# Kernel optimization log

Measured on AMD Instinct MI355X. Metric: run time of the kernel, lower is better.

## Reference

```python
import jax, jax.numpy as jnp
from jax import lax
import numpy as np

D_MODEL = 512
D_STATE = 16
DI = 1024        # expand * d_model
DT_RANK = 32     # ceil(d_model/16)
K = 4            # mamba d_conv
NC = 8           # n_clusters
B = 2
L = 1024
EPS_LN = 1e-5


def _ln(x, g, b):
    m = jnp.mean(x, axis=-1, keepdims=True)
    v = jnp.mean((x - m) ** 2, axis=-1, keepdims=True)
    return (x - m) / jnp.sqrt(v + EPS_LN) * g + b


def _l2norm(x):
    n = jnp.linalg.norm(x, axis=-1, keepdims=True)
    return x / jnp.maximum(n, 1e-12)


def _ssm_scan(dA, dBu, C):
    # dA, dBu: (B, L, DI, N); C: (B, L, N) -> y: (B, L, DI)
    def step(h, inp):
        dA_t, dBu_t, c_t = inp
        h = dA_t * h + dBu_t                      # (B, DI, N)
        y = jnp.einsum('bdn,bn->bd', h, c_t)      # (B, DI)
        return h, y
    h0 = jnp.zeros((dA.shape[0], dA.shape[2], dA.shape[3]), dA.dtype)
    _, ys = lax.scan(step, h0, (jnp.swapaxes(dA, 0, 1), jnp.swapaxes(dBu, 0, 1), jnp.swapaxes(C, 0, 1)))
    return jnp.swapaxes(ys, 0, 1)


def _mamba(x, in_w, conv_w, conv_b, xproj_w, dt_w, dt_b, A_log, Dp, out_w):
    # x: (B, L, d_model)
    xz = x @ in_w.T                               # (B, L, 2*DI)
    xp, z = jnp.split(xz, 2, axis=-1)
    # depthwise causal conv1d
    xc = lax.conv_general_dilated(jnp.swapaxes(xp, 1, 2), conv_w, (1,), [(K - 1, 0)], feature_group_count=DI)
    xc = jax.nn.silu(xc + conv_b[None, :, None])
    xc = jnp.swapaxes(xc, 1, 2)                   # (B, L, DI)
    x_dbl = xc @ xproj_w.T                        # (B, L, DT_RANK + 2*N)
    dt, Bm, Cm = jnp.split(x_dbl, [DT_RANK, DT_RANK + D_STATE], axis=-1)
    delta = jax.nn.softplus(dt @ dt_w.T + dt_b)   # (B, L, DI)
    A = -jnp.exp(A_log)                           # (DI, N)
    dA = jnp.exp(delta[..., None] * A)            # (B, L, DI, N)
    dBu = (delta * xc)[..., None] * Bm[:, :, None, :]
    y = _ssm_scan(dA, dBu, Cm) + xc * Dp
    y = y * jax.nn.silu(z)
    return y @ out_w.T


def _forward(x, norm1_g, norm1_b,
             fm_in_w, fm_conv_w, fm_conv_b, fm_xproj_w, fm_dt_w, fm_dt_b, fm_A_log, fm_D, fm_out_w,
             bm_in_w, bm_conv_w, bm_conv_b, bm_xproj_w, bm_dt_w, bm_dt_b, bm_A_log, bm_D, bm_out_w,
             fusion_w, fusion_b, cc_centers, cc_proj_w, cc_proj_b, cc_norm_g, cc_norm_b, cc_alpha,
             gate_w, gate_b, ffn_norm_g, ffn_norm_b, ffn_w1, ffn_b1, ffn_w2, ffn_b2):
    xn = _ln(x, norm1_g, norm1_b)
    # bidirectional mamba path
    f_out = _mamba(xn, fm_in_w, fm_conv_w, fm_conv_b, fm_xproj_w, fm_dt_w, fm_dt_b, fm_A_log, fm_D, fm_out_w)
    b_out = jnp.flip(_mamba(jnp.flip(xn, axis=1), bm_in_w, bm_conv_w, bm_conv_b, bm_xproj_w, bm_dt_w, bm_dt_b, bm_A_log, bm_D, bm_out_w), axis=1)
    mamba_out = jnp.concatenate([f_out, b_out], axis=-1) @ fusion_w.T + fusion_b
    # context clustering path (dropout = identity at eval)
    proj = xn @ cc_proj_w.T + cc_proj_b
    sim = jnp.einsum('bld,cd->blc', _l2norm(proj), _l2norm(cc_centers))
    w = jax.nn.softmax(sim, axis=-1)
    ctx = jnp.einsum('blc,cd->bld', w, cc_centers)
    cc_out = _ln(xn + cc_alpha * ctx, cc_norm_g, cc_norm_b)
    # gated fusion
    g = jax.nn.softmax(xn @ gate_w.T + gate_b, axis=-1)  # (B, L, 2)
    fused = g[..., 0:1] * mamba_out + g[..., 1:2] * cc_out
    x = x + fused
    h = _ln(x, ffn_norm_g, ffn_norm_b)
    h = jax.nn.gelu(h @ ffn_w1.T + ffn_b1, approximate=False) @ ffn_w2.T + ffn_b2
    return x + h


def setup_inputs() -> dict:
    key = jax.random.key(0)
    ks = iter(jax.random.split(key, 64))
    nrm = lambda shape, s=0.02: jax.random.normal(next(ks), shape, jnp.float32) * s

    def mamba_params():
        A_log = jnp.tile(jnp.log(jnp.arange(1, D_STATE + 1, dtype=jnp.float32))[None, :], (DI, 1))
        return dict(in_w=nrm((2 * DI, D_MODEL)), conv_w=nrm((DI, 1, K), 0.1), conv_b=jnp.zeros((DI,)),
                    xproj_w=nrm((DT_RANK + 2 * D_STATE, DI)), dt_w=nrm((DI, DT_RANK), 0.1),
                    dt_b=nrm((DI,), 0.1), A_log=A_log, D=jnp.ones((DI,)), out_w=nrm((D_MODEL, DI)))

    fm = mamba_params()
    bm = mamba_params()
    d = {
        'x': jax.random.normal(next(ks), (B, L, D_MODEL), jnp.float32),
        'norm1_g': jnp.ones((D_MODEL,)), 'norm1_b': jnp.zeros((D_MODEL,)),
        'fusion_w': nrm((D_MODEL, 2 * D_MODEL)), 'fusion_b': jnp.zeros((D_MODEL,)),
        'cc_centers': jax.random.normal(next(ks), (NC, D_MODEL), jnp.float32),
        'cc_proj_w': nrm((D_MODEL, D_MODEL)), 'cc_proj_b': jnp.zeros((D_MODEL,)),
        'cc_norm_g': jnp.ones((D_MODEL,)), 'cc_norm_b': jnp.zeros((D_MODEL,)),
        'cc_alpha': jnp.array([0.05], jnp.float32),
        'gate_w': nrm((2, D_MODEL)), 'gate_b': jnp.zeros((2,)),
        'ffn_norm_g': jnp.ones((D_MODEL,)), 'ffn_norm_b': jnp.zeros((D_MODEL,)),
        'ffn_w1': nrm((4 * D_MODEL, D_MODEL)), 'ffn_b1': jnp.zeros((4 * D_MODEL,)),
        'ffn_w2': nrm((D_MODEL, 4 * D_MODEL)), 'ffn_b2': jnp.zeros((D_MODEL,)),
    }
    for pfx, p in (('fm', fm), ('bm', bm)):
        for k, v in p.items():
            d[pfx + '_' + k] = v
    return d


def reference(x, norm1_g, norm1_b,
              fm_in_w, fm_conv_w, fm_conv_b, fm_xproj_w, fm_dt_w, fm_dt_b, fm_A_log, fm_D, fm_out_w,
              bm_in_w, bm_conv_w, bm_conv_b, bm_xproj_w, bm_dt_w, bm_dt_b, bm_A_log, bm_D, bm_out_w,
              fusion_w, fusion_b, cc_centers, cc_proj_w, cc_proj_b, cc_norm_g, cc_norm_b, cc_alpha,
              gate_w, gate_b, ffn_norm_g, ffn_norm_b, ffn_w1, ffn_b1, ffn_w2, ffn_b2):
    return _forward(x, norm1_g, norm1_b,
                    fm_in_w, fm_conv_w, fm_conv_b, fm_xproj_w, fm_dt_w, fm_dt_b, fm_A_log, fm_D, fm_out_w,
                    bm_in_w, bm_conv_w, bm_conv_b, bm_xproj_w, bm_dt_w, bm_dt_b, bm_A_log, bm_D, bm_out_w,
                    fusion_w, fusion_b, cc_centers, cc_proj_w, cc_proj_b, cc_norm_g, cc_norm_b, cc_alpha,
                    gate_w, gate_b, ffn_norm_g, ffn_norm_b, ffn_w1, ffn_b1, ffn_w2, ffn_b2)
```

## Files before the change

### kernel.cpp

```cpp
#include <hip/hip_runtime.h>
#include <hip/hip_bf16.h>
#include <hip/hip_fp16.h>
#include <math.h>

using bf16 = __hip_bfloat16;

typedef __attribute__((ext_vector_type(8))) short v8s;
typedef __attribute__((ext_vector_type(4))) short v4s;
typedef __attribute__((ext_vector_type(4))) float v4f;

constexpr int kB   = 2;
constexpr int kL   = 1024;
constexpr int kD   = 512;
constexpr int kDI  = 1024;
constexpr int kNS  = 16;
constexpr int kDTR = 32;
constexpr int kKC  = 4;
constexpr int kNC  = 8;
constexpr int kM   = kB * kL;
constexpr int kCH  = 32;
constexpr int kCL  = kL / kCH;
constexpr float kEPS = 1e-5f;

static __device__ __forceinline__ float toF(bf16 x) { return __bfloat162float(x); }
static __device__ __forceinline__ float b2f(short u) {
    unsigned int x = ((unsigned int)(unsigned short)u) << 16;
    return __uint_as_float(x);
}

static __device__ __forceinline__ float ldin(const void* p, int i, int f32) {
    if (f32) return ((const float*)p)[i];
    return toF(((const bf16*)p)[i]);
}

static __device__ __forceinline__ int flipL(int r) { return r ^ (kL - 1); }

__global__ void detect_kernel(const unsigned short* __restrict__ x, int* __restrict__ flag) {
    if (threadIdx.x == 0 && blockIdx.x == 0) {
        int plausible = 0;
        for (int i = 0; i < 512; ++i) {
            unsigned short h = x[2 * i];
            int e = (h >> 7) & 0xFF;
            if (e >= 100 && e <= 140) plausible++;
        }
        *flag = (plausible >= 256) ? 0 : 1;
    }
}

struct WSrcs { const void* p[12]; };

__global__ __launch_bounds__(256) void wconv_kernel(WSrcs s, bf16* __restrict__ dst,
                                                    const int* __restrict__ flg) {
    const int sz[12]  = {1048576, 1048576, 65536, 65536, 32768, 32768,
                         524288, 524288, 524288, 262144, 1048576, 1048576};
    const int off[12] = {0, 1048576, 2097152, 2162688, 2228224, 2260992,
                         2293760, 2818048, 3342336, 3866624, 4128768, 5177344};
    int t = blockIdx.y;
    int n = sz[t];
    const void* src = s.p[t];
    bf16* d = dst + off[t];
    int f32 = *flg;
    for (int i = blockIdx.x * 256 + threadIdx.x; i < n; i += gridDim.x * 256)
        d[i] = __float2bfloat16(ldin(src, i, f32));
}

__global__ __launch_bounds__(256) void an_kernel(const void* __restrict__ alog_f,
                                                 const void* __restrict__ alog_b,
                                                 float* __restrict__ anT,
                                                 const int* __restrict__ flg) {
    int f32 = *flg;
    int tid = blockIdx.x * 256 + threadIdx.x;
    int d = tid & (kDI - 1);
    int n = (tid >> 10) & (kNS - 1);
    int dir = tid >> 14;
    anT[tid] = -__expf(ldin(dir ? alog_b : alog_f, d * kNS + n, f32));
}

static __device__ __forceinline__ float blockReduceSum(float v, float* s) {
    __syncthreads();
#pragma unroll
    for (int o = 32; o > 0; o >>= 1) v += __shfl_down(v, o, 64);
    int lane = threadIdx.x & 63, wid = threadIdx.x >> 6;
    if (lane == 0) s[wid] = v;
    __syncthreads();
    if (threadIdx.x == 0) {
        float t = 0.f;
        for (int i = 0; i < 4; ++i) t += s[i];
        s[4] = t;
    }
    __syncthreads();
    return s[4];
}

__global__ __launch_bounds__(256) void ln_in_kernel(const void* __restrict__ X,
                                                    const void* __restrict__ g,
                                                    const void* __restrict__ b,
                                                    bf16* __restrict__ Y,
                                                    const int* __restrict__ flg) {
    __shared__ float sred[8];
    int f32 = *flg;
    int row = blockIdx.x;
    int i = threadIdx.x;
    size_t base = (size_t)row * kD;
    float x0 = ldin(X, base + i, f32), x1 = ldin(X, base + i + 256, f32);
    float mean = blockReduceSum(x0 + x1, sred) * (1.f / kD);
    float vs = blockReduceSum(x0 * x0 + x1 * x1, sred) * (1.f / kD) - mean * mean;
    float rstd = rsqrtf(vs + kEPS);
    Y[base + i]       = __float2bfloat16((x0 - mean) * rstd * ldin(g, i, f32)       + ldin(b, i, f32));
    Y[base + i + 256] = __float2bfloat16((x1 - mean) * rstd * ldin(g, i + 256, f32) + ldin(b, i + 256, f32));
}

__global__ __launch_bounds__(256) void ln_f32_kernel(const float* __restrict__ X,
                                                     const void* __restrict__ g,
                                                     const void* __restrict__ b,
                                                     bf16* __restrict__ Y,
                                                     const int* __restrict__ flg) {
    __shared__ float sred[8];
    int f32 = *flg;
    int row = blockIdx.x;
    int i = threadIdx.x;
    size_t base = (size_t)row * kD;
    float x0 = X[base + i], x1 = X[base + i + 256];
    float mean = blockReduceSum(x0 + x1, sred) * (1.f / kD);
    float vs = blockReduceSum(x0 * x0 + x1 * x1, sred) * (1.f / kD) - mean * mean;
    float rstd = rsqrtf(vs + kEPS);
    Y[base + i]       = __float2bfloat16((x0 - mean) * rstd * ldin(g, i, f32)       + ldin(b, i, f32));
    Y[base + i + 256] = __float2bfloat16((x1 - mean) * rstd * ldin(g, i + 256, f32) + ldin(b, i + 256, f32));
}

template <int BM, int BN, int WRN, int WCN>
__global__ __launch_bounds__(256) void mfma_gemm(const bf16* __restrict__ A, int lda, int aZOff,
                                                 const bf16* __restrict__ W, int K, int wZOff,
                                                 const void* __restrict__ bias, int act,
                                                 const float* __restrict__ resid,
                                                 bf16* __restrict__ outB,
                                                 void* __restrict__ outRaw,
                                                 int ldo, int oZOff,
                                                 int flipN0, int zflip,
                                                 const int* __restrict__ flg,
                                                 bf16* __restrict__ outSplitZ) {
    __shared__ bf16 As[BM * 64];
    __shared__ bf16 Bs[BN * 64];
    constexpr int FR = BM / WRN / 16;
    constexpr int FC = BN / WCN / 16;
    constexpr int AV = BM / 32;
    constexpr int BV = BN / 32;

    int f32 = *flg;
    int tid = threadIdx.x;
    int z = blockIdx.z;
    const bf16* Ab = A + (size_t)z * aZOff;
    const bf16* Wb = W + (size_t)z * wZOff;
    int m0 = blockIdx.y * BM, n0 = blockIdx.x * BN;
    int lane = tid & 63, w = tid >> 6;
    int wr = w % WRN, wc = w / WRN;
    int rbase = wr * (BM / WRN), cbase = wc * (BN / WCN);
    int quad = lane >> 4, lrow = lane & 15;
    int wbase = tid & ~63;

    v4f acc[FR][FC];
#pragma unroll
    for (int i = 0; i < FR; ++i)
#pragma unroll
        for (int j = 0; j < FC; ++j)
#pragma unroll
            for (int r = 0; r < 4; ++r) acc[i][j][r] = 0.f;

    for (int kt = 0; kt < K; kt += 64) {
#pragma unroll
        for (int i = 0; i < AV; ++i) {
            int v = i * 256 + tid;
            int row = v >> 3, c8 = (v & 7) * 8;
            const bf16* gp = Ab + (size_t)(m0 + row) * lda + kt + c8;
            __builtin_amdgcn_global_load_lds(
                (const __attribute__((address_space(1))) void*)gp,
                (__attribute__((address_space(3))) void*)&As[(i * 256 + wbase) * 8],
                16, 0, 0);
        }
#pragma unroll
        for (int i = 0; i < BV; ++i) {
            int v = i * 256 + tid;
            int row = v >> 3, c8 = (v & 7) * 8;
            const bf16* gp = Wb + (size_t)(n0 + row) * K + kt + c8;
            __builtin_amdgcn_global_load_lds(
                (const __attribute__((address_space(1))) void*)gp,
                (__attribute__((address_space(3))) void*)&Bs[(i * 256 + wbase) * 8],
                16, 0, 0);
        }
        __syncthreads();
#pragma unroll
        for (int k0 = 0; k0 < 64; k0 += 32) {
            v8s a[FR], b[FC];
#pragma unroll
            for (int fr = 0; fr < FR; ++fr)
                a[fr] = *reinterpret_cast<const v8s*>(&As[(rbase + fr * 16 + lrow) * 64 + k0 + quad * 8]);
#pragma unroll
            for (int fc = 0; fc < FC; ++fc)
                b[fc] = *reinterpret_cast<const v8s*>(&Bs[(cbase + fc * 16 + lrow) * 64 + k0 + quad * 8]);
#pragma unroll
            for (int fr = 0; fr < FR; ++fr)
#pragma unroll
                for (int fc = 0; fc < FC; ++fc)
                    acc[fr][fc] = __builtin_amdgcn_mfma_f32_16x16x32_bf16(a[fr], b[fc], acc[fr][fc], 0, 0, 0);
        }
        __syncthreads();
    }

    bf16* outBz = outB ? outB + (size_t)z * oZOff : nullptr;
#pragma unroll
    for (int fr = 0; fr < FR; ++fr) {
#pragma unroll
        for (int fc = 0; fc < FC; ++fc) {
            int ncol = n0 + cbase + fc * 16 + lrow;
            float bi = bias ? ldin(bias, ncol, f32) : 0.f;
            bool doflip = (ncol >= flipN0) || (zflip && z == 1);
#pragma unroll
            for (int r = 0; r < 4; ++r) {
                int m = m0 + rbase + fr * 16 + quad * 4 + r;
                float vv = acc[fr][fc][r] + bi;
                if (act == 2) vv = 0.5f * vv * (1.f + erff(vv * 0.70710678118654752440f));
                if (resid) vv += resid[(size_t)m * ldo + ncol];
                if (outSplitZ) {
                    int dir = (ncol >> 11) & 1;
                    int isz = (ncol >> 10) & 1;
                    int c2 = dir * 1024 + (ncol & 1023);
                    int mo_ = dir ? flipL(m) : m;
                    bf16* dst = isz ? outSplitZ : outB;
                    dst[(size_t)mo_ * 2048 + c2] = __float2bfloat16(vv);
                } else {
                    int mo_ = doflip ? flipL(m) : m;
                    size_t oi = (size_t)mo_ * ldo + ncol;
                    if (outBz) outBz[oi] = __float2bfloat16(vv);
                    else if (f32) ((float*)outRaw)[oi] = vv;
                    else ((bf16*)outRaw)[oi] = __float2bfloat16(vv);
                }
            }
        }
    }
}

__global__ __launch_bounds__(256) void conv_kernel(const bf16* __restrict__ xp,
                                                   const void* __restrict__ cw_f,
                                                   const void* __restrict__ cb_f,
                                                   const void* __restrict__ cw_b,
                                                   const void* __restrict__ cb_b,
                                                   bf16* __restrict__ xc,
                                                   const int* __restrict__ flg) {
    int f32 = *flg;
    int tid = blockIdx.x * 256 + threadIdx.x;
    int d = tid & (kDI - 1);
    int r = (tid >> 10) & (kM - 1);
    int dir = tid >> 21;
    int l = r & (kL - 1);
    int b = r >> 10;
    const void* cw = dir ? cw_b : cw_f;
    const void* cb = dir ? cb_b : cb_f;
    float acc = ldin(cb, d, f32);
#pragma unroll
    for (int k = 0; k < kKC; ++k) {
        int ll = l - (kKC - 1) + k;
        if (ll >= 0)
            acc += ldin(cw, d * kKC + k, f32) *
                   toF(xp[(size_t)(b * kL + ll) * (2 * kDI) + dir * kDI + d]);
    }
    float s = acc / (1.f + __expf(-acc));
    xc[(size_t)r * (2 * kDI) + dir * kDI + d] = __float2bfloat16(s);
}

__global__ __launch_bounds__(256) void delta_kernel(const bf16* __restrict__ xdbl,
                                                    const bf16* __restrict__ wdt,
                                                    const void* __restrict__ dtb_f,
                                                    const void* __restrict__ dtb_b,
                                                    __half* __restrict__ deltaH,
                                                    const int* __restrict__ flg) {
    __shared__ float arow[kDTR];
    int f32 = *flg;
    int m = blockIdx.y;
    int dir = blockIdx.z;
    int d = blockIdx.x * 256 + threadIdx.x;
    if (threadIdx.x < kDTR)
        arow[threadIdx.x] = toF(xdbl[(size_t)m * 128 + dir * 64 + threadIdx.x]);
    __syncthreads();
    float acc = ldin(dir ? dtb_b : dtb_f, d, f32);
    const v8s* wv = reinterpret_cast<const v8s*>(wdt + ((size_t)dir * kDI + d) * kDTR);
#pragma unroll
    for (int t = 0; t < 4; ++t) {
        v8s w8 = wv[t];
#pragma unroll
        for (int k = 0; k < 8; ++k) acc += arow[t * 8 + k] * b2f(w8[k]);
    }
    acc = (acc > 20.f) ? acc : log1pf(__expf(acc));
    deltaH[((size_t)dir * kM + m) * kDI + d] = __float2half(acc);
}

__global__ __launch_bounds__(256) void scan_phase1(const bf16* __restrict__ xc,
                                                   const bf16* __restrict__ xdbl,
                                                   __half* __restrict__ deltaS,
                                                   const float* __restrict__ anT,
                                                   float* __restrict__ PA,
                                                   __half* __restrict__ HLh,
                                                   bf16* __restrict__ ymul,
                                                   const int* __restrict__ flg) {
    int tid = blockIdx.x * 256 + threadIdx.x;
    int n4  = tid & 3;
    int d   = (tid >> 2) & (kDI - 1);
    int c   = (tid >> 12) & (kCH - 1);
    int b   = (tid >> 17) & 1;
    int dir = tid >> 18;
    float an[4], h[4], pa[4];
#pragma unroll
    for (int j = 0; j < 4; ++j) {
        an[j] = anT[((size_t)dir * kNS + n4 * 4 + j) * kDI + d];
        h[j] = 0.f;
        pa[j] = 1.f;
    }
    __half* dptr = deltaS + ((size_t)dir * kM + (size_t)b * kL) * kDI + d;
    float s = 0.f;
    int l0 = c * kCL;
    for (int l = l0; l < l0 + kCL; ++l) {
        size_t rb = (size_t)b * kL + l;
        float dl = __half2float(dptr[(size_t)l * kDI]);
        s += dl;
        float xcv = toF(xc[rb * (2 * kDI) + dir * kDI + d]);
        float du = dl * xcv;
        v4s Bv = *reinterpret_cast<const v4s*>(xdbl + rb * 128 + dir * 64 + kDTR + n4 * 4);
        v4s Cv = *reinterpret_cast<const v4s*>(xdbl + rb * 128 + dir * 64 + kDTR + kNS + n4 * 4);
        float yp = 0.f;
#pragma unroll
        for (int j = 0; j < 4; ++j) {
            float a = __expf(dl * an[j]);
            pa[j] *= a;
            h[j] = a * h[j] + du * b2f(Bv[j]);
            yp += h[j] * b2f(Cv[j]);
        }
        yp += __shfl_xor(yp, 1);
        yp += __shfl_xor(yp, 2);
        if (n4 == 0) {
            ymul[rb * (2 * kDI) + dir * kDI + d] = __float2bfloat16(yp);
            dptr[(size_t)l * kDI] = __float2half(s);
        }
    }
    int g = dir * kB + b;
    size_t o = (((size_t)g * kCH + c) * kNS + n4 * 4) * kDI + d;
#pragma unroll
    for (int j = 0; j < 4; ++j) {
        PA[o + (size_t)j * kDI] = pa[j];
        HLh[o + (size_t)j * kDI] = __float2half(h[j]);
    }
}

__global__ __launch_bounds__(256) void scan_phase2(float* __restrict__ PA,
                                                   const __half* __restrict__ HLh) {
    int tid = blockIdx.x * 256 + threadIdx.x;
    int d = tid & (kDI - 1);
    int n = (tid >> 10) & (kNS - 1);
    int g = tid >> 14;
    float h = 0.f;
    for (int c = 0; c < kCH; ++c) {
        size_t idx = (((size_t)g * kCH + c) * kNS + n) * kDI + d;
        float pav = PA[idx];
        float hlv = __half2float(HLh[idx]);
        PA[idx] = h;
        h = pav * h + hlv;
    }
}

__global__ __launch_bounds__(256) void scan_fix(const bf16* __restrict__ xc,
                                                const bf16* __restrict__ xdbl,
                                                const bf16* __restrict__ zb,
                                                const __half* __restrict__ sbuf,
                                                const float* __restrict__ anT,
                                                const void* __restrict__ dp_f,
                                                const void* __restrict__ dp_b,
                                                const float* __restrict__ HIN,
                                                bf16* __restrict__ ymul,
                                                const int* __restrict__ flg) {
    int f32 = *flg;
    int tid = blockIdx.x * 256 + threadIdx.x;
    int d   = tid & (kDI - 1);
    int l   = (tid >> 10) & (kL - 1);
    int b   = (tid >> 20) & 1;
    int dir = tid >> 21;
    int c   = l / kCL;
    size_t rb = (size_t)b * kL + l;
    float s = __half2float(sbuf[((size_t)dir * kM + rb) * kDI + d]);
    int g = dir * kB + b;
    const float* hin = HIN + (((size_t)g * kCH + c) * kNS) * kDI + d;
    const float* anp = anT + (size_t)dir * kNS * kDI + d;
    const bf16* Cp = xdbl + rb * 128 + dir * 64 + kDTR + kNS;
    float ycorr = 0.f;
#pragma unroll
    for (int n = 0; n < kNS; ++n) {
        float an = anp[(size_t)n * kDI];
        ycorr += toF(Cp[n]) * __expf(an * s) * hin[(size_t)n * kDI];
    }
    size_t yi = rb * (2 * kDI) + dir * kDI + d;
    float xcv = toF(xc[yi]);
    float Dv = ldin(dir ? dp_b : dp_f, d, f32);
    float y = toF(ymul[yi]) + ycorr + xcv * Dv;
    float zv = toF(zb[yi]);
    float sz = zv / (1.f + __expf(-zv));
    ymul[yi] = __float2bfloat16(y * sz);
}

__global__ void cnorm_kernel(const void* __restrict__ C, float* __restrict__ cn,
                             const int* __restrict__ flg) {
    int f32 = *flg;
    int c = blockIdx.x;
    int lane = threadIdx.x;
    float s = 0.f;
    for (int i = lane; i < kD; i += 64) {
        float v = ldin(C, c * kD + i, f32);
        s += v * v;
    }
#pragma unroll
    for (int o = 32; o > 0; o >>= 1) s += __shfl_down(s, o, 64);
    if (lane == 0) cn[c] = sqrtf(s);
}

__global__ __launch_bounds__(256) void cc_kernel(const bf16* __restrict__ proj,
                                                 const void* __restrict__ centers,
                                                 const float* __restrict__ cn,
                                                 const bf16* __restrict__ xn,
                                                 const void* __restrict__ alpha_p,
                                                 const void* __restrict__ g,
                                                 const void* __restrict__ bb,
                                                 bf16* __restrict__ ccout,
                                                 const int* __restrict__ flg) {
    __shared__ float sred[8];
    __shared__ float sims[kNC];
    int f32 = *flg;
    int row = blockIdx.x;
    int i = threadIdx.x;
    size_t base = (size_t)row * kD;
    float p0 = toF(proj[base + i]), p1 = toF(proj[base + i + 256]);
    float sumsq = blockReduceSum(p0 * p0 + p1 * p1, sred);
    float pn = fmaxf(sqrtf(sumsq), 1e-12f);
    for (int c = 0; c < kNC; ++c) {
        float part = p0 * ldin(centers, c * kD + i, f32) + p1 * ldin(centers, c * kD + i + 256, f32);
        float dot = blockReduceSum(part, sred);
        if (threadIdx.x == 0) sims[c] = dot / (pn * fmaxf(cn[c], 1e-12f));
    }
    __syncthreads();
    float mx = -1e30f;
#pragma unroll
    for (int c = 0; c < kNC; ++c) mx = fmaxf(mx, sims[c]);
    float wv[kNC], se = 0.f;
#pragma unroll
    for (int c = 0; c < kNC; ++c) { wv[c] = __expf(sims[c] - mx); se += wv[c]; }
    float inv = 1.f / se;
    float ctx0 = 0.f, ctx1 = 0.f;
#pragma unroll
    for (int c = 0; c < kNC; ++c) {
        float wc = wv[c] * inv;
        ctx0 += wc * ldin(centers, c * kD + i, f32);
        ctx1 += wc * ldin(centers, c * kD + i + 256, f32);
    }
    float alpha = ldin(alpha_p, 0, f32);
    float t0 = toF(xn[base + i]) + alpha * ctx0;
    float t1 = toF(xn[base + i + 256]) + alpha * ctx1;
    float mean = blockReduceSum(t0 + t1, sred) * (1.f / kD);
    float vs = blockReduceSum(t0 * t0 + t1 * t1, sred) * (1.f / kD) - mean * mean;
    float rstd = rsqrtf(vs + kEPS);
    ccout[base + i]       = __float2bfloat16((t0 - mean) * rstd * ldin(g, i, f32)       + ldin(bb, i, f32));
    ccout[base + i + 256] = __float2bfloat16((t1 - mean) * rstd * ldin(g, i + 256, f32) + ldin(bb, i + 256, f32));
}

__global__ __launch_bounds__(256) void gate_kernel(const bf16* __restrict__ xn,
                                                   const void* __restrict__ X,
                                                   const bf16* __restrict__ mo,
                                                   const bf16* __restrict__ cc,
                                                   const void* __restrict__ gw,
                                                   const void* __restrict__ gb,
                                                   float* __restrict__ xmid,
                                                   const int* __restrict__ flg) {
    __shared__ float sred[8];
    int f32 = *flg;
    int row = blockIdx.x;
    int i = threadIdx.x;
    size_t base = (size_t)row * kD;
    float x0 = toF(xn[base + i]), x1 = toF(xn[base + i + 256]);
    float d0 = blockReduceSum(x0 * ldin(gw, i, f32) + x1 * ldin(gw, i + 256, f32), sred);
    float d1 = blockReduceSum(x0 * ldin(gw, kD + i, f32) + x1 * ldin(gw, kD + i + 256, f32), sred);
    d0 += ldin(gb, 0, f32);
    d1 += ldin(gb, 1, f32);
    float mx = fmaxf(d0, d1);
    float e0 = __expf(d0 - mx), e1 = __expf(d1 - mx);
    float s = e0 + e1;
    float g0 = e0 / s, g1 = e1 / s;
    xmid[base + i]       = ldin(X, base + i, f32)       + g0 * toF(mo[base + i])       + g1 * toF(cc[base + i]);
    xmid[base + i + 256] = ldin(X, base + i + 256, f32) + g0 * toF(mo[base + i + 256]) + g1 * toF(cc[base + i + 256]);
}

extern "C" void kernel_launch(void* const* d_in, const int* in_sizes, int n_in,
                              void* d_out, int out_size, void* d_ws, size_t ws_size,
                              hipStream_t stream) {
    bool sig = (n_in > 3 && in_sizes[3] == 2 * kDI * kD);
    int I_fusion_w = sig ? 21 : 3,  I_fusion_b = sig ? 22 : 4;
    int I_centers  = sig ? 23 : 5,  I_ccp_w    = sig ? 24 : 6,  I_ccp_b = sig ? 25 : 7;
    int I_ccn_g    = sig ? 26 : 8,  I_ccn_b    = sig ? 27 : 9,  I_alpha = sig ? 28 : 10;
    int I_gate_w   = sig ? 29 : 11, I_gate_b   = sig ? 30 : 12;
    int I_ffn_g    = sig ? 31 : 13, I_ffn_b    = sig ? 32 : 14;
    int I_ffn_w1   = sig ? 33 : 15, I_ffn_b1   = sig ? 34 : 16;
    int I_ffn_w2   = sig ? 35 : 17, I_ffn_b2   = sig ? 36 : 18;
    int I_fm       = sig ? 3  : 19, I_bm       = sig ? 12 : 28;

    const void* X        = d_in[0];
    const void* n1g      = d_in[1];
    const void* n1b      = d_in[2];
    const void* fusion_b = d_in[I_fusion_b];
    const void* centers  = d_in[I_centers];
    const void* ccp_b    = d_in[I_ccp_b];
    const void* ccn_g    = d_in[I_ccn_g];
    const void* ccn_b    = d_in[I_ccn_b];
    const void* cc_alpha = d_in[I_alpha];
    const void* gate_w   = d_in[I_gate_w];
    const void* gate_b   = d_in[I_gate_b];
    const void* ffn_g    = d_in[I_ffn_g];
    const void* ffn_b    = d_in[I_ffn_b];
    const void* ffn_b1   = d_in[I_ffn_b1];
    const void* ffn_b2   = d_in[I_ffn_b2];

    float* ws = (float*)d_ws;
    int* flg  = (int*)d_ws;
    float* cn = ws + 8;
    float*  anT  = ws + 32;
    float*  PA   = anT + 32768;
    __half* HLh  = (__half*)(PA + 2097152);
    bf16*  xn   = (bf16*)((float*)HLh + 1048576);
    bf16*  xp   = (bf16*)((float*)xn + 524288);
    bf16*  zb   = (bf16*)((float*)xp + 2097152);
    bf16*  xc   = (bf16*)((float*)zb + 2097152);
    bf16*  xdbl = (bf16*)((float*)xc + 2097152);
    bf16*  ymul = (bf16*)((float*)xdbl + 131072);
    bf16*  wbuf = (bf16*)((float*)ymul + 2097152);
    __half* deltaH = (__half*)xp;
    bf16*  fb    = (bf16*)HLh;
    bf16*  mo    = (bf16*)PA;
    float* xmid  = PA + 524288;
    bf16*  hln   = xc;
    bf16*  ffnh  = zb;
    bf16*  ccout = ymul;
    bf16*  projb = fb;

    bf16* w_in     = wbuf + 0;
    bf16* w_xp     = wbuf + 2097152;
    bf16* w_dt     = wbuf + 2228224;
    bf16* w_out    = wbuf + 2293760;
    bf16* w_fusion = wbuf + 3342336;
    bf16* w_ccp    = wbuf + 3866624;
    bf16* w_ffn1   = wbuf + 4128768;
    bf16* w_ffn2   = wbuf + 5177344;

    dim3 blk(256);
    constexpr int NOFLIP = 1 << 30;

    detect_kernel<<<1, 64, 0, stream>>>((const unsigned short*)X, flg);

    WSrcs srcs;
    srcs.p[0] = d_in[I_fm + 0]; srcs.p[1] = d_in[I_bm + 0];
    srcs.p[2] = d_in[I_fm + 3]; srcs.p[3] = d_in[I_bm + 3];
    srcs.p[4] = d_in[I_fm + 4]; srcs.p[5] = d_in[I_bm + 4];
    srcs.p[6] = d_in[I_fm + 8]; srcs.p[7] = d_in[I_bm + 8];
    srcs.p[8] = d_in[I_fusion_w]; srcs.p[9] = d_in[I_ccp_w];
    srcs.p[10] = d_in[I_ffn_w1]; srcs.p[11] = d_in[I_ffn_w2];
    wconv_kernel<<<dim3(512, 12), blk, 0, stream>>>(srcs, wbuf, flg);

    an_kernel<<<128, blk, 0, stream>>>(d_in[I_fm + 6], d_in[I_bm + 6], anT, flg);

    ln_in_kernel<<<kM, blk, 0, stream>>>(X, n1g, n1b, xn, flg);

    mfma_gemm<128, 128, 2, 2><<<dim3(32, 16, 1), blk, 0, stream>>>(
        xn, kD, 0, w_in, kD, 0, nullptr, 0, nullptr, xp, nullptr, 2048, 0, NOFLIP, 0, flg, zb);

    conv_kernel<<<2 * kM * kDI / 256, blk, 0, stream>>>(
        xp, d_in[I_fm + 1], d_in[I_fm + 2], d_in[I_bm + 1], d_in[I_bm + 2], xc, flg);

    mfma_gemm<64, 64, 2, 2><<<dim3(1, 32, 2), blk, 0, stream>>>(
        xc, 2 * kDI, kDI, w_xp, kDI, 65536, nullptr, 0, nullptr, xdbl, nullptr, 128, 64,
        NOFLIP, 0, flg, nullptr);

    delta_kernel<<<dim3(kDI / 256, kM, 2), blk, 0, stream>>>(
        xdbl, w_dt, d_in[I_fm + 5], d_in[I_bm + 5], deltaH, flg);

    scan_phase1<<<2048, blk, 0, stream>>>(xc, xdbl, deltaH, anT, PA, HLh, ymul, flg);
    scan_phase2<<<256, blk, 0, stream>>>(PA, HLh);
    scan_fix<<<16384, blk, 0, stream>>>(xc, xdbl, zb, deltaH, anT,
                                        d_in[I_fm + 7], d_in[I_bm + 7], PA, ymul, flg);

    mfma_gemm<64, 64, 2, 2><<<dim3(8, 32, 2), blk, 0, stream>>>(
        ymul, 2 * kDI, kDI, w_out, kDI, 524288, nullptr, 0, nullptr, fb, nullptr, 2 * kD, kD,
        NOFLIP, 1, flg, nullptr);

    mfma_gemm<64, 64, 2, 2><<<dim3(8, 32, 1), blk, 0, stream>>>(
        fb, 2 * kD, 0, w_fusion, 2 * kD, 0, fusion_b, 0, nullptr, mo, nullptr, kD, 0,
        NOFLIP, 0, flg, nullptr);

    mfma_gemm<64, 64, 2, 2><<<dim3(8, 32, 1), blk, 0, stream>>>(
        xn, kD, 0, w_ccp, kD, 0, ccp_b, 0, nullptr, projb, nullptr, kD, 0, NOFLIP, 0, flg,
        nullptr);
    cnorm_kernel<<<kNC, 64, 0, stream>>>(centers, cn, flg);
    cc_kernel<<<kM, blk, 0, stream>>>(projb, centers, cn, xn, cc_alpha, ccn_g, ccn_b, ccout, flg);

    gate_kernel<<<kM, blk, 0, stream>>>(xn, X, mo, ccout, gate_w, gate_b, xmid, flg);

    ln_f32_kernel<<<kM, blk, 0, stream>>>(xmid, ffn_g, ffn_b, hln, flg);
    mfma_gemm<128, 64, 2, 2><<<dim3(32, 16, 1), blk, 0, stream>>>(
        hln, kD, 0, w_ffn1, kD, 0, ffn_b1, 2, nullptr, ffnh, nullptr, 4 * kD, 0, NOFLIP, 0, flg,
        nullptr);
    mfma_gemm<64, 64, 2, 2><<<dim3(8, 32, 1), blk, 0, stream>>>(
        ffnh, 4 * kD, 0, w_ffn2, 4 * kD, 0, ffn_b2, 0, xmid, nullptr, d_out, kD, 0,
        NOFLIP, 0, flg, nullptr);
}
```

Measured before the change: 435.6 us.

## Fuse cluster-context, gate and FFN layernorm kernels; shrink GEMM tiles; parallelize detect

```diff
diff --git a/kernel.cpp b/kernel.cpp
--- a/kernel.cpp
+++ b/kernel.cpp
@@ -36,15 +36,16 @@
 static __device__ __forceinline__ int flipL(int r) { return r ^ (kL - 1); }
 
 __global__ void detect_kernel(const unsigned short* __restrict__ x, int* __restrict__ flag) {
-    if (threadIdx.x == 0 && blockIdx.x == 0) {
-        int plausible = 0;
-        for (int i = 0; i < 512; ++i) {
-            unsigned short h = x[2 * i];
-            int e = (h >> 7) & 0xFF;
-            if (e >= 100 && e <= 140) plausible++;
-        }
-        *flag = (plausible >= 256) ? 0 : 1;
-    }
+    int lane = threadIdx.x;
+    int cnt = 0;
+    for (int i = lane; i < 512; i += 64) {
+        unsigned short h = x[2 * i];
+        int e = (h >> 7) & 0xFF;
+        if (e >= 100 && e <= 140) cnt++;
+    }
+#pragma unroll
+    for (int o = 32; o > 0; o >>= 1) cnt += __shfl_down(cnt, o, 64);
+    if (lane == 0) *flag = (cnt >= 256) ? 0 : 1;
 }
 
 struct WSrcs { const void* p[12]; };
@@ -103,24 +104,6 @@
     int i = threadIdx.x;
     size_t base = (size_t)row * kD;
     float x0 = ldin(X, base + i, f32), x1 = ldin(X, base + i + 256, f32);
-    float mean = blockReduceSum(x0 + x1, sred) * (1.f / kD);
-    float vs = blockReduceSum(x0 * x0 + x1 * x1, sred) * (1.f / kD) - mean * mean;
-    float rstd = rsqrtf(vs + kEPS);
-    Y[base + i]       = __float2bfloat16((x0 - mean) * rstd * ldin(g, i, f32)       + ldin(b, i, f32));
-    Y[base + i + 256] = __float2bfloat16((x1 - mean) * rstd * ldin(g, i + 256, f32) + ldin(b, i + 256, f32));
-}
-
-__global__ __launch_bounds__(256) void ln_f32_kernel(const float* __restrict__ X,
-                                                     const void* __restrict__ g,
-                                                     const void* __restrict__ b,
-                                                     bf16* __restrict__ Y,
-                                                     const int* __restrict__ flg) {
-    __shared__ float sred[8];
-    int f32 = *flg;
-    int row = blockIdx.x;
-    int i = threadIdx.x;
-    size_t base = (size_t)row * kD;
-    float x0 = X[base + i], x1 = X[base + i + 256];
     float mean = blockReduceSum(x0 + x1, sred) * (1.f / kD);
     float vs = blockReduceSum(x0 * x0 + x1 * x1, sred) * (1.f / kD) - mean * mean;
     float rstd = rsqrtf(vs + kEPS);
@@ -418,15 +401,22 @@
     if (lane == 0) cn[c] = sqrtf(s);
 }
 
-__global__ __launch_bounds__(256) void cc_kernel(const bf16* __restrict__ proj,
-                                                 const void* __restrict__ centers,
-                                                 const float* __restrict__ cn,
-                                                 const bf16* __restrict__ xn,
-                                                 const void* __restrict__ alpha_p,
-                                                 const void* __restrict__ g,
-                                                 const void* __restrict__ bb,
-                                                 bf16* __restrict__ ccout,
-                                                 const int* __restrict__ flg) {
+__global__ __launch_bounds__(256) void post_kernel(const bf16* __restrict__ proj,
+                                                   const void* __restrict__ centers,
+                                                   const float* __restrict__ cn,
+                                                   const bf16* __restrict__ xn,
+                                                   const void* __restrict__ alpha_p,
+                                                   const void* __restrict__ ccg,
+                                                   const void* __restrict__ ccb,
+                                                   const void* __restrict__ X,
+                                                   const bf16* __restrict__ mo,
+                                                   const void* __restrict__ gw,
+                                                   const void* __restrict__ gb,
+                                                   const void* __restrict__ fg,
+                                                   const void* __restrict__ fbb,
+                                                   float* __restrict__ xmid,
+                                                   bf16* __restrict__ hln,
+                                                   const int* __restrict__ flg) {
     __shared__ float sred[8];
     __shared__ float sims[kNC];
     int f32 = *flg;
@@ -457,39 +447,31 @@
         ctx1 += wc * ldin(centers, c * kD + i + 256, f32);
     }
     float alpha = ldin(alpha_p, 0, f32);
-    float t0 = toF(xn[base + i]) + alpha * ctx0;
-    float t1 = toF(xn[base + i + 256]) + alpha * ctx1;
+    float x0 = toF(xn[base + i]), x1 = toF(xn[base + i + 256]);
+    float t0 = x0 + alpha * ctx0;
+    float t1 = x1 + alpha * ctx1;
     float mean = blockReduceSum(t0 + t1, sred) * (1.f / kD);
     float vs = blockReduceSum(t0 * t0 + t1 * t1, sred) * (1.f / kD) - mean * mean;
     float rstd = rsqrtf(vs + kEPS);
-    ccout[base + i]       = __float2bfloat16((t0 - mean) * rstd * ldin(g, i, f32)       + ldin(bb, i, f32));
-    ccout[base + i + 256] = __float2bfloat16((t1 - mean) * rstd * ldin(g, i + 256, f32) + ldin(bb, i + 256, f32));
-}
-
-__global__ __launch_bounds__(256) void gate_kernel(const bf16* __restrict__ xn,
-                                                   const void* __restrict__ X,
-                                                   const bf16* __restrict__ mo,
-                                                   const bf16* __restrict__ cc,
-                                                   const void* __restrict__ gw,
-                                                   const void* __restrict__ gb,
-                                                   float* __restrict__ xmid,
-                                                   const int* __restrict__ flg) {
-    __shared__ float sred[8];
-    int f32 = *flg;
-    int row = blockIdx.x;
-    int i = threadIdx.x;
-    size_t base = (size_t)row * kD;
-    float x0 = toF(xn[base + i]), x1 = toF(xn[base + i + 256]);
+    float cc0 = (t0 - mean) * rstd * ldin(ccg, i, f32)       + ldin(ccb, i, f32);
+    float cc1 = (t1 - mean) * rstd * ldin(ccg, i + 256, f32) + ldin(ccb, i + 256, f32);
     float d0 = blockReduceSum(x0 * ldin(gw, i, f32) + x1 * ldin(gw, i + 256, f32), sred);
     float d1 = blockReduceSum(x0 * ldin(gw, kD + i, f32) + x1 * ldin(gw, kD + i + 256, f32), sred);
     d0 += ldin(gb, 0, f32);
     d1 += ldin(gb, 1, f32);
-    float mx = fmaxf(d0, d1);
-    float e0 = __expf(d0 - mx), e1 = __expf(d1 - mx);
-    float s = e0 + e1;
-    float g0 = e0 / s, g1 = e1 / s;
-    xmid[base + i]       = ldin(X, base + i, f32)       + g0 * toF(mo[base + i])       + g1 * toF(cc[base + i]);
-    xmid[base + i + 256] = ldin(X, base + i + 256, f32) + g0 * toF(mo[base + i + 256]) + g1 * toF(cc[base + i + 256]);
+    float gmx = fmaxf(d0, d1);
+    float e0 = __expf(d0 - gmx), e1 = __expf(d1 - gmx);
+    float gs = e0 + e1;
+    float g0 = e0 / gs, g1 = e1 / gs;
+    float xm0 = ldin(X, base + i, f32)       + g0 * toF(mo[base + i])       + g1 * cc0;
+    float xm1 = ldin(X, base + i + 256, f32) + g0 * toF(mo[base + i + 256]) + g1 * cc1;
+    xmid[base + i] = xm0;
+    xmid[base + i + 256] = xm1;
+    float mean2 = blockReduceSum(xm0 + xm1, sred) * (1.f / kD);
+    float vs2 = blockReduceSum(xm0 * xm0 + xm1 * xm1, sred) * (1.f / kD) - mean2 * mean2;
+    float rstd2 = rsqrtf(vs2 + kEPS);
+    hln[base + i]       = __float2bfloat16((xm0 - mean2) * rstd2 * ldin(fg, i, f32)       + ldin(fbb, i, f32));
+    hln[base + i + 256] = __float2bfloat16((xm1 - mean2) * rstd2 * ldin(fg, i + 256, f32) + ldin(fbb, i + 256, f32));
 }
 
 extern "C" void kernel_launch(void* const* d_in, const int* in_sizes, int n_in,
@@ -540,7 +522,6 @@
     float* xmid  = PA + 524288;
     bf16*  hln   = xc;
     bf16*  ffnh  = zb;
-    bf16*  ccout = ymul;
     bf16*  projb = fb;
 
     bf16* w_in     = wbuf + 0;
@@ -570,13 +551,13 @@
 
     ln_in_kernel<<<kM, blk, 0, stream>>>(X, n1g, n1b, xn, flg);
 
-    mfma_gemm<128, 128, 2, 2><<<dim3(32, 16, 1), blk, 0, stream>>>(
+    mfma_gemm<128, 64, 2, 2><<<dim3(64, 16, 1), blk, 0, stream>>>(
         xn, kD, 0, w_in, kD, 0, nullptr, 0, nullptr, xp, nullptr, 2048, 0, NOFLIP, 0, flg, zb);
 
     conv_kernel<<<2 * kM * kDI / 256, blk, 0, stream>>>(
         xp, d_in[I_fm + 1], d_in[I_fm + 2], d_in[I_bm + 1], d_in[I_bm + 2], xc, flg);
 
-    mfma_gemm<64, 64, 2, 2><<<dim3(1, 32, 2), blk, 0, stream>>>(
+    mfma_gemm<32, 64, 1, 4><<<dim3(1, 64, 2), blk, 0, stream>>>(
         xc, 2 * kDI, kDI, w_xp, kDI, 65536, nullptr, 0, nullptr, xdbl, nullptr, 128, 64,
         NOFLIP, 0, flg, nullptr);
 
@@ -588,27 +569,26 @@
     scan_fix<<<16384, blk, 0, stream>>>(xc, xdbl, zb, deltaH, anT,
                                         d_in[I_fm + 7], d_in[I_bm + 7], PA, ymul, flg);
 
-    mfma_gemm<64, 64, 2, 2><<<dim3(8, 32, 2), blk, 0, stream>>>(
+    mfma_gemm<32, 64, 1, 4><<<dim3(8, 64, 2), blk, 0, stream>>>(
         ymul, 2 * kDI, kDI, w_out, kDI, 524288, nullptr, 0, nullptr, fb, nullptr, 2 * kD, kD,
         NOFLIP, 1, flg, nullptr);
 
-    mfma_gemm<64, 64, 2, 2><<<dim3(8, 32, 1), blk, 0, stream>>>(
+    mfma_gemm<32, 64, 1, 4><<<dim3(8, 64, 1), blk, 0, stream>>>(
         fb, 2 * kD, 0, w_fusion, 2 * kD, 0, fusion_b, 0, nullptr, mo, nullptr, kD, 0,
         NOFLIP, 0, flg, nullptr);
 
-    mfma_gemm<64, 64, 2, 2><<<dim3(8, 32, 1), blk, 0, stream>>>(
+    mfma_gemm<32, 64, 1, 4><<<dim3(8, 64, 1), blk, 0, stream>>>(
         xn, kD, 0, w_ccp, kD, 0, ccp_b, 0, nullptr, projb, nullptr, kD, 0, NOFLIP, 0, flg,
         nullptr);
     cnorm_kernel<<<kNC, 64, 0, stream>>>(centers, cn, flg);
-    cc_kernel<<<kM, blk, 0, stream>>>(projb, centers, cn, xn, cc_alpha, ccn_g, ccn_b, ccout, flg);
-
-    gate_kernel<<<kM, blk, 0, stream>>>(xn, X, mo, ccout, gate_w, gate_b, xmid, flg);
-
-    ln_f32_kernel<<<kM, blk, 0, stream>>>(xmid, ffn_g, ffn_b, hln, flg);
-    mfma_gemm<128, 64, 2, 2><<<dim3(32, 16, 1), blk, 0, stream>>>(
+
+    post_kernel<<<kM, blk, 0, stream>>>(projb, centers, cn, xn, cc_alpha, ccn_g, ccn_b,
+                                        X, mo, gate_w, gate_b, ffn_g, ffn_b, xmid, hln, flg);
+
+    mfma_gemm<64, 64, 2, 2><<<dim3(32, 32, 1), blk, 0, stream>>>(
         hln, kD, 0, w_ffn1, kD, 0, ffn_b1, 2, nullptr, ffnh, nullptr, 4 * kD, 0, NOFLIP, 0, flg,
         nullptr);
-    mfma_gemm<64, 64, 2, 2><<<dim3(8, 32, 1), blk, 0, stream>>>(
+    mfma_gemm<32, 64, 1, 4><<<dim3(8, 64, 1), blk, 0, stream>>>(
         ffnh, 4 * kD, 0, w_ffn2, 4 * kD, 0, ffn_b2, 0, xmid, nullptr, d_out, kD, 0,
         NOFLIP, 0, flg, nullptr);
 }
```

Result: faster. 389.2 us (-10.7%).
